# Optimization experiments

Measured on AMD Instinct MI355X. Metric: run time of the kernel, lower is better.

Reference implementation:

```python
import jax, jax.numpy as jnp
import numpy as np

DIM = 2048        # model hidden size
INTER = 1408      # per-expert intermediate size
E = 16            # n_routed_experts
TOPK = 2          # n_activated_experts
S_INTER = 2816    # shared experts intermediate (n_shared_experts * INTER)
T = 4096          # tokens (batch*seq, module flattens to [-1, dim])
ROUTE_SCALE = 1.0


def setup_inputs() -> dict:
    key = jax.random.key(0)
    ks = jax.random.split(key, 8)
    g = lambda k, shape, scale: (jax.random.normal(k, shape, dtype=jnp.float32) * scale)
    return {
        "x": g(ks[0], (T, DIM), 1.0),
        "gate_w": g(ks[1], (E, DIM), 0.02),
        "w1": g(ks[2], (E, INTER, DIM), 0.02),
        "w2": g(ks[3], (E, DIM, INTER), 0.02),
        "w3": g(ks[4], (E, INTER, DIM), 0.02),
        "sw1": g(ks[5], (S_INTER, DIM), 0.02),
        "sw2": g(ks[6], (DIM, S_INTER), 0.02),
        "sw3": g(ks[7], (S_INTER, DIM), 0.02),
    }


def _moe_forward(x, gate_w, w1, w2, w3, sw1, sw2, sw3):
    t = x.shape[0]
    # ---- gate: softmax scores -> top-k experts per token ----
    scores = jax.nn.softmax(x @ gate_w.T, axis=-1)          # [T, E]
    top_w, top_i = jax.lax.top_k(scores, TOPK)              # [T, K]
    top_w = top_w * ROUTE_SCALE
    # dense combine weights [T, E]: zero for unselected experts
    combine = jnp.zeros((t, E), x.dtype).at[jnp.arange(t)[:, None], top_i].add(top_w)
    # ---- routed experts: gated silu MLP per expert, weighted combine ----
    # loop over the small fixed expert count; tokens with combine==0 contribute 0,
    # matching the original scatter/gather dispatch math exactly.
    y = jnp.zeros_like(x)
    for e in range(E):
        h = jax.nn.silu(x @ w1[e].T) * (x @ w3[e].T)        # [T, INTER]
        y = y + (h @ w2[e].T) * combine[:, e:e + 1]
    # ---- shared experts ----
    z = (jax.nn.silu(x @ sw1.T) * (x @ sw3.T)) @ sw2.T      # [T, DIM]
    return y + z


def reference(x, gate_w, w1, w2, w3, sw1, sw2, sw3):
    return _moe_forward(x, gate_w, w1, w2, w3, sw1, sw2, sw3)
```

## Files before the change

kernel.cpp:

```cpp
#include <hip/hip_runtime.h>
#include <hip/hip_bf16.h>
#include <cstdint>
#include <cstddef>

#define TTOK   4096
#define DIM_   2048
#define INTER_ 1408
#define NEXP   16
#define SINTER_ 2816
#define BM 128
#define BN 128
#define BK 32
#define MAXROWS (TTOK*2 + NEXP*BM)
#define MAXMT   (TTOK*2/BM + NEXP)

typedef unsigned short u16;
typedef __attribute__((ext_vector_type(8))) short short8;
typedef __attribute__((ext_vector_type(4))) float f32x4;

#define AS3P(p) ((__attribute__((address_space(3))) void*)(p))
#define AS1P(p) ((const __attribute__((address_space(1))) void*)(p))

__device__ __forceinline__ void gll16(const void* g, void* l) {
    __builtin_amdgcn_global_load_lds(AS1P(g), AS3P(l), 16, 0, 0);
}

__device__ __forceinline__ u16 f2bf(float f) {
    __hip_bfloat16 h = __float2bfloat16(f);
    union { __hip_bfloat16 h; u16 u; } c; c.h = h; return c.u;
}

__device__ __forceinline__ unsigned pk2(float a, float b) {
    unsigned r;
    asm("v_cvt_pk_bf16_f32 %0, %1, %2" : "=v"(r) : "v"(a), "v"(b));
    return r;
}

__device__ __forceinline__ int4 pack8(float4 a, float4 b) {
    int4 r;
    r.x = (int)pk2(a.x, a.y);
    r.y = (int)pk2(a.z, a.w);
    r.z = (int)pk2(b.x, b.y);
    r.w = (int)pk2(b.z, b.w);
    return r;
}


__global__ void init_kernel(int* perm_rt, float* pw_rt, int* perm_sh, int* misc, int* zrow) {
    int i = blockIdx.x * 256 + threadIdx.x;
    if (i < MAXROWS) { perm_rt[i] = -1; pw_rt[i] = 0.f; }
    if (i < TTOK)    perm_sh[i] = i;
    if (i < 32)      misc[i] = 0;
    if (i < 1024)    zrow[i] = 0;
}

__global__ void cvt_kernel(const float* __restrict__ s, u16* __restrict__ d, int n8) {
    int stride = gridDim.x * 256;
    for (int i = blockIdx.x * 256 + threadIdx.x; i < n8; i += stride) {
        const float4* s4 = (const float4*)(s + (size_t)i * 8);
        float4 a = s4[0], b = s4[1];
        *(int4*)(d + (size_t)i * 8) = pack8(a, b);
    }
}

__global__ void gate_kernel(const float* __restrict__ x, const float* __restrict__ gw,
                            int* __restrict__ topi, float* __restrict__ topw,
                            int* __restrict__ misc) {
    int t = blockIdx.x;
    int lane = threadIdx.x;
    const float* xr = x + (size_t)t * DIM_;
    float acc[NEXP];
#pragma unroll
    for (int e = 0; e < NEXP; e++) acc[e] = 0.f;
#pragma unroll
    for (int i = 0; i < 8; i++) {
        int k = i * 256 + lane * 4;
        float4 xv = *(const float4*)(xr + k);
#pragma unroll
        for (int e = 0; e < NEXP; e++) {
            float4 gv = *(const float4*)(gw + (size_t)e * DIM_ + k);
            acc[e] += xv.x * gv.x + xv.y * gv.y + xv.z * gv.z + xv.w * gv.w;
        }
    }
#pragma unroll
    for (int e = 0; e < NEXP; e++) {
        float v = acc[e];
        for (int off = 32; off > 0; off >>= 1) v += __shfl_down(v, off);
        acc[e] = v;
    }
    if (lane == 0) {
        float m = acc[0];
#pragma unroll
        for (int e = 1; e < NEXP; e++) m = fmaxf(m, acc[e]);
        float p[NEXP]; float s = 0.f;
#pragma unroll
        for (int e = 0; e < NEXP; e++) { p[e] = __expf(acc[e] - m); s += p[e]; }
        int i0 = 0; float v0 = p[0];
#pragma unroll
        for (int e = 1; e < NEXP; e++) if (p[e] > v0) { v0 = p[e]; i0 = e; }
        int i1 = -1; float v1 = -1.f;
#pragma unroll
        for (int e = 0; e < NEXP; e++) if (e != i0 && p[e] > v1) { v1 = p[e]; i1 = e; }
        float inv = 1.f / s;
        topi[2 * t] = i0; topi[2 * t + 1] = i1;
        topw[2 * t] = v0 * inv; topw[2 * t + 1] = v1 * inv;
        atomicAdd(&misc[i0], 1);
        atomicAdd(&misc[i1], 1);
    }
}

__global__ void scan_kernel(int* misc) {
    int* counts = misc;
    int* base   = misc + 32;
    int* te     = misc + 48;
    int* tr     = misc + 128;
    int b = 0, tt = 0;
    for (int e = 0; e < NEXP; e++) {
        int c = counts[e];
        int nt = (c + BM - 1) >> 7;
        base[e] = b;
        for (int i = 0; i < nt; i++) { te[tt] = e; tr[tt] = b + i * BM; tt++; }
        b += nt * BM;
    }
    for (int i = tt; i < MAXMT; i++) te[i] = -1;
}

__global__ void scatter_kernel(const int* __restrict__ topi, const float* __restrict__ topw,
                               int* __restrict__ misc, int* __restrict__ perm,
                               float* __restrict__ pw) {
    int t = blockIdx.x * 256 + threadIdx.x;
    if (t >= TTOK) return;
    int* fill = misc + 16;
    int* base = misc + 32;
#pragma unroll
    for (int k = 0; k < 2; k++) {
        int e = topi[2 * t + k];
        int pos = base[e] + atomicAdd(&fill[e], 1);
        perm[pos] = t;
        pw[pos] = topw[2 * t + k];
    }
}


template<bool GROUPED>
__global__ __launch_bounds__(256, 2) void gemm_h13_k(
    const u16* __restrict__ Xb,
    const u16* __restrict__ W1b, const u16* __restrict__ W3b,
    u16* __restrict__ H,
    const int* __restrict__ perm,
    const int* __restrict__ te, const int* __restrict__ tr,
    const u16* __restrict__ zrow,
    int N, int K, int nt_m, int chunk)
{
    const int q = (blockIdx.x & 7) * chunk + (blockIdx.x >> 3);
    if (q >= nt_m * (N / BN)) return;
    const int jn = q / nt_m, im = q % nt_m;
    int e, slot0;
    if (GROUPED) { e = te[im]; if (e < 0) return; slot0 = tr[im]; }
    else         { e = 0; slot0 = im * BM; }
    const int n0 = jn * BN;
    const u16* W1 = W1b + (size_t)e * N * K;
    const u16* W3 = W3b + (size_t)e * N * K;

    __shared__ __align__(16) u16 As[BM * BK];
    __shared__ __align__(16) u16 B1s[BM * BK];
    __shared__ __align__(16) u16 B3s[BM * BK];

    const int tid = threadIdx.x;
    const int lane = tid & 63, wid = tid >> 6;
    const int wr = wid >> 1, wc = wid & 1;
    const int col = lane & 15, kg = lane >> 4;

    const int lr = lane >> 2;
    const int kb = ((lane & 3) ^ ((lane >> 3) & 3)) * 8;
    const int ar0 = wid * 32 + lr, ar1 = ar0 + 16;
    const int ta0 = perm[slot0 + ar0];
    const int ta1 = perm[slot0 + ar1];
    const u16* ga0 = (ta0 >= 0 ? Xb + (size_t)ta0 * K : zrow) + kb;
    const u16* ga1 = (ta1 >= 0 ? Xb + (size_t)ta1 * K : zrow) + kb;
    const u16* gb1a = W1 + (size_t)(n0 + ar0) * K + kb;
    const u16* gb1b = W1 + (size_t)(n0 + ar1) * K + kb;
    const u16* gb3a = W3 + (size_t)(n0 + ar0) * K + kb;
    const u16* gb3b = W3 + (size_t)(n0 + ar1) * K + kb;
    u16* la0 = As  + (wid * 32) * BK;
    u16* la1 = As  + (wid * 32 + 16) * BK;
    u16* lb1a = B1s + (wid * 32) * BK;
    u16* lb1b = B1s + (wid * 32 + 16) * BK;
    u16* lb3a = B3s + (wid * 32) * BK;
    u16* lb3b = B3s + (wid * 32 + 16) * BK;

    const int sw = (col >> 1) & 3;

    f32x4 acc1[4][4] = {};
    f32x4 acc3[4][4] = {};

    for (int k0 = 0; k0 < K; k0 += BK) {
        gll16(ga0 + k0, la0);
        gll16(ga1 + k0, la1);
        gll16(gb1a + k0, lb1a);
        gll16(gb1b + k0, lb1b);
        gll16(gb3a + k0, lb3a);
        gll16(gb3b + k0, lb3b);
        __syncthreads();

        short8 a[4];
#pragma unroll
        for (int mi = 0; mi < 4; mi++)
            a[mi] = *(const short8*)(As + (wr * 64 + mi * 16 + col) * BK + ((kg ^ sw) * 8));
#pragma unroll
        for (int ni = 0; ni < 4; ni++) {
            const int rowB = (wc * 64 + ni * 16 + col) * BK + ((kg ^ sw) * 8);
            short8 v1 = *(const short8*)(B1s + rowB);
            short8 v3 = *(const short8*)(B3s + rowB);
#pragma unroll
            for (int mi = 0; mi < 4; mi++) {
                acc1[mi][ni] = __builtin_amdgcn_mfma_f32_16x16x32_bf16(a[mi], v1, acc1[mi][ni], 0, 0, 0);
                acc3[mi][ni] = __builtin_amdgcn_mfma_f32_16x16x32_bf16(a[mi], v3, acc3[mi][ni], 0, 0, 0);
            }
        }
        __syncthreads();
    }

#pragma unroll
    for (int mi = 0; mi < 4; mi++) {
#pragma unroll
        for (int j = 0; j < 4; j++) {
            int row = slot0 + wr * 64 + mi * 16 + kg * 4 + j;
#pragma unroll
            for (int ni = 0; ni < 4; ni++) {
                float v1 = acc1[mi][ni][j];
                float v3 = acc3[mi][ni][j];
                float hv = v1 / (1.f + __expf(-v1)) * v3;
                int c = n0 + wc * 64 + ni * 16 + col;
                H[(size_t)row * N + c] = f2bf(hv);
            }
        }
    }
}

template<bool ATOMIC>
__global__ __launch_bounds__(256, 2) void gemm_out_k(
    const u16* __restrict__ Hm,
    const u16* __restrict__ W2b,
    float* __restrict__ Out,
    const int* __restrict__ perm, const float* __restrict__ pw,
    const int* __restrict__ te, const int* __restrict__ tr,
    int K, int nt_m, int chunk)
{
    const int q = (blockIdx.x & 7) * chunk + (blockIdx.x >> 3);
    if (q >= nt_m * (DIM_ / BN)) return;
    const int jn = q / nt_m, im = q % nt_m;
    int e, slot0;
    if (ATOMIC) { e = te[im]; if (e < 0) return; slot0 = tr[im]; }
    else        { e = 0; slot0 = im * BM; }
    const int n0 = jn * BN;
    const u16* W2 = W2b + (size_t)e * DIM_ * K;

    __shared__ __align__(16) u16 As[BM * BK];
    __shared__ __align__(16) u16 Bs[BM * BK];

    const int tid = threadIdx.x;
    const int lane = tid & 63, wid = tid >> 6;
    const int wr = wid >> 1, wc = wid & 1;
    const int col = lane & 15, kg = lane >> 4;

    const int lr = lane >> 2;
    const int kb = ((lane & 3) ^ ((lane >> 3) & 3)) * 8;
    const int ar0 = wid * 32 + lr, ar1 = ar0 + 16;
    const u16* ga0 = Hm + (size_t)(slot0 + ar0) * K + kb;
    const u16* ga1 = Hm + (size_t)(slot0 + ar1) * K + kb;
    const u16* gb0 = W2 + (size_t)(n0 + ar0) * K + kb;
    const u16* gb1 = W2 + (size_t)(n0 + ar1) * K + kb;
    u16* la0 = As + (wid * 32) * BK;
    u16* la1 = As + (wid * 32 + 16) * BK;
    u16* lb0 = Bs + (wid * 32) * BK;
    u16* lb1 = Bs + (wid * 32 + 16) * BK;

    const int sw = (col >> 1) & 3;

    f32x4 acc[4][4] = {};

    for (int k0 = 0; k0 < K; k0 += BK) {
        gll16(ga0 + k0, la0);
        gll16(ga1 + k0, la1);
        gll16(gb0 + k0, lb0);
        gll16(gb1 + k0, lb1);
        __syncthreads();

        short8 a[4];
#pragma unroll
        for (int mi = 0; mi < 4; mi++)
            a[mi] = *(const short8*)(As + (wr * 64 + mi * 16 + col) * BK + ((kg ^ sw) * 8));
#pragma unroll
        for (int ni = 0; ni < 4; ni++) {
            short8 bv = *(const short8*)(Bs + (wc * 64 + ni * 16 + col) * BK + ((kg ^ sw) * 8));
#pragma unroll
            for (int mi = 0; mi < 4; mi++)
                acc[mi][ni] = __builtin_amdgcn_mfma_f32_16x16x32_bf16(a[mi], bv, acc[mi][ni], 0, 0, 0);
        }
        __syncthreads();
    }

#pragma unroll
    for (int mi = 0; mi < 4; mi++) {
#pragma unroll
        for (int j = 0; j < 4; j++) {
            int rloc = wr * 64 + mi * 16 + kg * 4 + j;
            int slot = slot0 + rloc;
            if (ATOMIC) {
                int token = perm[slot];
                if (token < 0) continue;
                float w = pw[slot];
#pragma unroll
                for (int ni = 0; ni < 4; ni++) {
                    int c = n0 + wc * 64 + ni * 16 + col;
                    atomicAdd(&Out[(size_t)token * DIM_ + c], acc[mi][ni][j] * w);
                }
            } else {
#pragma unroll
                for (int ni = 0; ni < 4; ni++) {
                    int c = n0 + wc * 64 + ni * 16 + col;
                    Out[(size_t)slot * DIM_ + c] = acc[mi][ni][j];
                }
            }
        }
    }
}


extern "C" void kernel_launch(void* const* d_in, const int* in_sizes, int n_in,
                              void* d_out, int out_size, void* d_ws, size_t ws_size,
                              hipStream_t stream) {
    (void)in_sizes; (void)n_in; (void)out_size; (void)ws_size;
    const float* x   = (const float*)d_in[0];
    const float* gw  = (const float*)d_in[1];
    const float* w1  = (const float*)d_in[2];
    const float* w2  = (const float*)d_in[3];
    const float* w3  = (const float*)d_in[4];
    const float* sw1 = (const float*)d_in[5];
    const float* sw2 = (const float*)d_in[6];
    const float* sw3 = (const float*)d_in[7];
    float* out = (float*)d_out;

    char* ws = (char*)d_ws;
    size_t off = 0;
    auto take = [&](size_t bytes) -> void* {
        void* p = ws + off;
        off += (bytes + 255) & ~(size_t)255;
        return p;
    };
    u16*   xb      = (u16*)take((size_t)TTOK * DIM_ * 2);
    u16*   hbuf    = (u16*)take((size_t)MAXROWS * INTER_ * 2);
    int*   perm_rt = (int*)take((size_t)MAXROWS * 4);
    float* pw_rt   = (float*)take((size_t)MAXROWS * 4);
    int*   perm_sh = (int*)take((size_t)TTOK * 4);
    int*   topi    = (int*)take((size_t)TTOK * 2 * 4);
    float* topw    = (float*)take((size_t)TTOK * 2 * 4);
    int*   misc    = (int*)take(1024);
    int*   zrow    = (int*)take(4096);
    const size_t nW  = (size_t)NEXP * INTER_ * DIM_;
    const size_t nSW = (size_t)SINTER_ * DIM_;
    u16* w1b  = (u16*)take(nW * 2);
    u16* w2b  = (u16*)take(nW * 2);
    u16* w3b  = (u16*)take(nW * 2);
    u16* sw1b = (u16*)take(nSW * 2);
    u16* sw2b = (u16*)take(nSW * 2);
    u16* sw3b = (u16*)take(nSW * 2);

    init_kernel<<<MAXROWS / 256, 256, 0, stream>>>(perm_rt, pw_rt, perm_sh, misc, zrow);
    cvt_kernel<<<2048, 256, 0, stream>>>(x, xb, TTOK * DIM_ / 8);
    gate_kernel<<<TTOK, 64, 0, stream>>>(x, gw, topi, topw, misc);
    scan_kernel<<<1, 1, 0, stream>>>(misc);
    scatter_kernel<<<TTOK / 256, 256, 0, stream>>>(topi, topw, misc, perm_rt, pw_rt);

    cvt_kernel<<<4096, 256, 0, stream>>>(w1,  w1b,  (int)(nW / 8));
    cvt_kernel<<<4096, 256, 0, stream>>>(w2,  w2b,  (int)(nW / 8));
    cvt_kernel<<<4096, 256, 0, stream>>>(w3,  w3b,  (int)(nW / 8));
    cvt_kernel<<<4096, 256, 0, stream>>>(sw1, sw1b, (int)(nSW / 8));
    cvt_kernel<<<4096, 256, 0, stream>>>(sw2, sw2b, (int)(nSW / 8));
    cvt_kernel<<<4096, 256, 0, stream>>>(sw3, sw3b, (int)(nSW / 8));

    auto grid8 = [](int total) { return ((total + 7) / 8) * 8; };
    auto chunk8 = [](int total) { return (total + 7) / 8; };

    {
        int total = (TTOK / BM) * (SINTER_ / BN);
        gemm_h13_k<false><<<grid8(total), 256, 0, stream>>>(
            xb, sw1b, sw3b, hbuf, perm_sh, nullptr, nullptr, (const u16*)zrow,
            SINTER_, DIM_, TTOK / BM, chunk8(total));
    }
    {
        int total = (TTOK / BM) * (DIM_ / BN);
        gemm_out_k<false><<<grid8(total), 256, 0, stream>>>(
            hbuf, sw2b, out, nullptr, nullptr, nullptr, nullptr,
            SINTER_, TTOK / BM, chunk8(total));
    }
    {
        int total = MAXMT * (INTER_ / BN);
        gemm_h13_k<true><<<grid8(total), 256, 0, stream>>>(
            xb, w1b, w3b, hbuf, perm_rt, misc + 48, misc + 128, (const u16*)zrow,
            INTER_, DIM_, MAXMT, chunk8(total));
    }
    {
        int total = MAXMT * (DIM_ / BN);
        gemm_out_k<true><<<grid8(total), 256, 0, stream>>>(
            hbuf, w2b, out, perm_rt, pw_rt, misc + 48, misc + 128,
            INTER_, MAXMT, chunk8(total));
    }
}
```

Before: 864.0 us.

## Split fused W1/W3 gate GEMM into two single-B GEMMs with bf16 intermediate

```diff
diff --git a/kernel.cpp b/kernel.cpp
--- a/kernel.cpp
+++ b/kernel.cpp
@@ -30,6 +30,10 @@
     union { __hip_bfloat16 h; u16 u; } c; c.h = h; return c.u;
 }
 
+__device__ __forceinline__ float bf2f(u16 u) {
+    return __uint_as_float((unsigned)u << 16);
+}
+
 __device__ __forceinline__ unsigned pk2(float a, float b) {
     unsigned r;
     asm("v_cvt_pk_bf16_f32 %0, %1, %2" : "=v"(r) : "v"(a), "v"(b));
@@ -46,10 +50,9 @@
 }
 
 
-__global__ void init_kernel(int* perm_rt, float* pw_rt, int* perm_sh, int* misc, int* zrow) {
+__global__ void init_kernel(int* perm_rt, float* pw_rt, int* misc, int* zrow) {
     int i = blockIdx.x * 256 + threadIdx.x;
     if (i < MAXROWS) { perm_rt[i] = -1; pw_rt[i] = 0.f; }
-    if (i < TTOK)    perm_sh[i] = i;
     if (i < 32)      misc[i] = 0;
     if (i < 1024)    zrow[i] = 0;
 }
@@ -142,12 +145,11 @@
 }
 
 
-template<bool GROUPED>
-__global__ __launch_bounds__(256, 2) void gemm_h13_k(
-    const u16* __restrict__ Xb,
-    const u16* __restrict__ W1b, const u16* __restrict__ W3b,
-    u16* __restrict__ H,
-    const int* __restrict__ perm,
+template<bool GROUPED, int EPI>
+__global__ __launch_bounds__(256, 3) void gemm_s(
+    const u16* __restrict__ A, const u16* __restrict__ B,
+    const u16* __restrict__ T1, u16* __restrict__ OutB, float* __restrict__ OutF,
+    const int* __restrict__ perm, const float* __restrict__ pw,
     const int* __restrict__ te, const int* __restrict__ tr,
     const u16* __restrict__ zrow,
     int N, int K, int nt_m, int chunk)
@@ -159,12 +161,10 @@
     if (GROUPED) { e = te[im]; if (e < 0) return; slot0 = tr[im]; }
     else         { e = 0; slot0 = im * BM; }
     const int n0 = jn * BN;
-    const u16* W1 = W1b + (size_t)e * N * K;
-    const u16* W3 = W3b + (size_t)e * N * K;
+    const u16* Bw = B + (size_t)e * N * K;
 
     __shared__ __align__(16) u16 As[BM * BK];
-    __shared__ __align__(16) u16 B1s[BM * BK];
-    __shared__ __align__(16) u16 B3s[BM * BK];
+    __shared__ __align__(16) u16 Bs[BM * BK];
 
     const int tid = threadIdx.x;
     const int lane = tid & 63, wid = tid >> 6;
@@ -174,103 +174,19 @@
     const int lr = lane >> 2;
     const int kb = ((lane & 3) ^ ((lane >> 3) & 3)) * 8;
     const int ar0 = wid * 32 + lr, ar1 = ar0 + 16;
-    const int ta0 = perm[slot0 + ar0];
-    const int ta1 = perm[slot0 + ar1];
-    const u16* ga0 = (ta0 >= 0 ? Xb + (size_t)ta0 * K : zrow) + kb;
-    const u16* ga1 = (ta1 >= 0 ? Xb + (size_t)ta1 * K : zrow) + kb;
-    const u16* gb1a = W1 + (size_t)(n0 + ar0) * K + kb;
-    const u16* gb1b = W1 + (size_t)(n0 + ar1) * K + kb;
-    const u16* gb3a = W3 + (size_t)(n0 + ar0) * K + kb;
-    const u16* gb3b = W3 + (size_t)(n0 + ar1) * K + kb;
-    u16* la0 = As  + (wid * 32) * BK;
-    u16* la1 = As  + (wid * 32 + 16) * BK;
-    u16* lb1a = B1s + (wid * 32) * BK;
-    u16* lb1b = B1s + (wid * 32 + 16) * BK;
-    u16* lb3a = B3s + (wid * 32) * BK;
-    u16* lb3b = B3s + (wid * 32 + 16) * BK;
-
-    const int sw = (col >> 1) & 3;
-
-    f32x4 acc1[4][4] = {};
-    f32x4 acc3[4][4] = {};
-
-    for (int k0 = 0; k0 < K; k0 += BK) {
-        gll16(ga0 + k0, la0);
-        gll16(ga1 + k0, la1);
-        gll16(gb1a + k0, lb1a);
-        gll16(gb1b + k0, lb1b);
-        gll16(gb3a + k0, lb3a);
-        gll16(gb3b + k0, lb3b);
-        __syncthreads();
-
-        short8 a[4];
-#pragma unroll
-        for (int mi = 0; mi < 4; mi++)
-            a[mi] = *(const short8*)(As + (wr * 64 + mi * 16 + col) * BK + ((kg ^ sw) * 8));
-#pragma unroll
-        for (int ni = 0; ni < 4; ni++) {
-            const int rowB = (wc * 64 + ni * 16 + col) * BK + ((kg ^ sw) * 8);
-            short8 v1 = *(const short8*)(B1s + rowB);
-            short8 v3 = *(const short8*)(B3s + rowB);
-#pragma unroll
-            for (int mi = 0; mi < 4; mi++) {
-                acc1[mi][ni] = __builtin_amdgcn_mfma_f32_16x16x32_bf16(a[mi], v1, acc1[mi][ni], 0, 0, 0);
-                acc3[mi][ni] = __builtin_amdgcn_mfma_f32_16x16x32_bf16(a[mi], v3, acc3[mi][ni], 0, 0, 0);
-            }
-        }
-        __syncthreads();
-    }
-
-#pragma unroll
-    for (int mi = 0; mi < 4; mi++) {
-#pragma unroll
-        for (int j = 0; j < 4; j++) {
-            int row = slot0 + wr * 64 + mi * 16 + kg * 4 + j;
-#pragma unroll
-            for (int ni = 0; ni < 4; ni++) {
-                float v1 = acc1[mi][ni][j];
-                float v3 = acc3[mi][ni][j];
-                float hv = v1 / (1.f + __expf(-v1)) * v3;
-                int c = n0 + wc * 64 + ni * 16 + col;
-                H[(size_t)row * N + c] = f2bf(hv);
-            }
-        }
-    }
-}
-
-template<bool ATOMIC>
-__global__ __launch_bounds__(256, 2) void gemm_out_k(
-    const u16* __restrict__ Hm,
-    const u16* __restrict__ W2b,
-    float* __restrict__ Out,
-    const int* __restrict__ perm, const float* __restrict__ pw,
-    const int* __restrict__ te, const int* __restrict__ tr,
-    int K, int nt_m, int chunk)
-{
-    const int q = (blockIdx.x & 7) * chunk + (blockIdx.x >> 3);
-    if (q >= nt_m * (DIM_ / BN)) return;
-    const int jn = q / nt_m, im = q % nt_m;
-    int e, slot0;
-    if (ATOMIC) { e = te[im]; if (e < 0) return; slot0 = tr[im]; }
-    else        { e = 0; slot0 = im * BM; }
-    const int n0 = jn * BN;
-    const u16* W2 = W2b + (size_t)e * DIM_ * K;
-
-    __shared__ __align__(16) u16 As[BM * BK];
-    __shared__ __align__(16) u16 Bs[BM * BK];
-
-    const int tid = threadIdx.x;
-    const int lane = tid & 63, wid = tid >> 6;
-    const int wr = wid >> 1, wc = wid & 1;
-    const int col = lane & 15, kg = lane >> 4;
-
-    const int lr = lane >> 2;
-    const int kb = ((lane & 3) ^ ((lane >> 3) & 3)) * 8;
-    const int ar0 = wid * 32 + lr, ar1 = ar0 + 16;
-    const u16* ga0 = Hm + (size_t)(slot0 + ar0) * K + kb;
-    const u16* ga1 = Hm + (size_t)(slot0 + ar1) * K + kb;
-    const u16* gb0 = W2 + (size_t)(n0 + ar0) * K + kb;
-    const u16* gb1 = W2 + (size_t)(n0 + ar1) * K + kb;
+    const u16* ga0;
+    const u16* ga1;
+    if (GROUPED && EPI < 2) {
+        const int ta0 = perm[slot0 + ar0];
+        const int ta1 = perm[slot0 + ar1];
+        ga0 = (ta0 >= 0 ? A + (size_t)ta0 * K : zrow) + kb;
+        ga1 = (ta1 >= 0 ? A + (size_t)ta1 * K : zrow) + kb;
+    } else {
+        ga0 = A + (size_t)(slot0 + ar0) * K + kb;
+        ga1 = A + (size_t)(slot0 + ar1) * K + kb;
+    }
+    const u16* gb0 = Bw + (size_t)(n0 + ar0) * K + kb;
+    const u16* gb1 = Bw + (size_t)(n0 + ar1) * K + kb;
     u16* la0 = As + (wid * 32) * BK;
     u16* la1 = As + (wid * 32 + 16) * BK;
     u16* lb0 = Bs + (wid * 32) * BK;
@@ -307,20 +223,35 @@
         for (int j = 0; j < 4; j++) {
             int rloc = wr * 64 + mi * 16 + kg * 4 + j;
             int slot = slot0 + rloc;
-            if (ATOMIC) {
+            if (EPI == 0) {
+#pragma unroll
+                for (int ni = 0; ni < 4; ni++) {
+                    float v = acc[mi][ni][j];
+                    float s = v / (1.f + __expf(-v));
+                    int c = n0 + wc * 64 + ni * 16 + col;
+                    OutB[(size_t)slot * N + c] = f2bf(s);
+                }
+            } else if (EPI == 1) {
+#pragma unroll
+                for (int ni = 0; ni < 4; ni++) {
+                    int c = n0 + wc * 64 + ni * 16 + col;
+                    float s1 = bf2f(T1[(size_t)slot * N + c]);
+                    OutB[(size_t)slot * N + c] = f2bf(s1 * acc[mi][ni][j]);
+                }
+            } else if (EPI == 2) {
+#pragma unroll
+                for (int ni = 0; ni < 4; ni++) {
+                    int c = n0 + wc * 64 + ni * 16 + col;
+                    OutF[(size_t)slot * DIM_ + c] = acc[mi][ni][j];
+                }
+            } else {
                 int token = perm[slot];
                 if (token < 0) continue;
                 float w = pw[slot];
 #pragma unroll
                 for (int ni = 0; ni < 4; ni++) {
                     int c = n0 + wc * 64 + ni * 16 + col;
-                    atomicAdd(&Out[(size_t)token * DIM_ + c], acc[mi][ni][j] * w);
-                }
-            } else {
-#pragma unroll
-                for (int ni = 0; ni < 4; ni++) {
-                    int c = n0 + wc * 64 + ni * 16 + col;
-                    Out[(size_t)slot * DIM_ + c] = acc[mi][ni][j];
+                    atomicAdd(&OutF[(size_t)token * DIM_ + c], acc[mi][ni][j] * w);
                 }
             }
         }
@@ -349,11 +280,13 @@
         off += (bytes + 255) & ~(size_t)255;
         return p;
     };
+    const size_t nT1 = (size_t)MAXROWS * INTER_;
+    const size_t nHB = (nT1 > (size_t)TTOK * SINTER_) ? nT1 : (size_t)TTOK * SINTER_;
     u16*   xb      = (u16*)take((size_t)TTOK * DIM_ * 2);
-    u16*   hbuf    = (u16*)take((size_t)MAXROWS * INTER_ * 2);
+    u16*   t1buf   = (u16*)take(nHB * 2);
+    u16*   hbuf    = (u16*)take(nHB * 2);
     int*   perm_rt = (int*)take((size_t)MAXROWS * 4);
     float* pw_rt   = (float*)take((size_t)MAXROWS * 4);
-    int*   perm_sh = (int*)take((size_t)TTOK * 4);
     int*   topi    = (int*)take((size_t)TTOK * 2 * 4);
     float* topw    = (float*)take((size_t)TTOK * 2 * 4);
     int*   misc    = (int*)take(1024);
@@ -367,7 +300,7 @@
     u16* sw2b = (u16*)take(nSW * 2);
     u16* sw3b = (u16*)take(nSW * 2);
 
-    init_kernel<<<MAXROWS / 256, 256, 0, stream>>>(perm_rt, pw_rt, perm_sh, misc, zrow);
+    init_kernel<<<MAXROWS / 256, 256, 0, stream>>>(perm_rt, pw_rt, misc, zrow);
     cvt_kernel<<<2048, 256, 0, stream>>>(x, xb, TTOK * DIM_ / 8);
     gate_kernel<<<TTOK, 64, 0, stream>>>(x, gw, topi, topw, misc);
     scan_kernel<<<1, 1, 0, stream>>>(misc);
@@ -383,28 +316,36 @@
     auto grid8 = [](int total) { return ((total + 7) / 8) * 8; };
     auto chunk8 = [](int total) { return (total + 7) / 8; };
 
+    const int ntm_sh = TTOK / BM;
+
     {
-        int total = (TTOK / BM) * (SINTER_ / BN);
-        gemm_h13_k<false><<<grid8(total), 256, 0, stream>>>(
-            xb, sw1b, sw3b, hbuf, perm_sh, nullptr, nullptr, (const u16*)zrow,
-            SINTER_, DIM_, TTOK / BM, chunk8(total));
+        int total = ntm_sh * (SINTER_ / BN);
+        gemm_s<false, 0><<<grid8(total), 256, 0, stream>>>(
+            xb, sw1b, nullptr, t1buf, nullptr, nullptr, nullptr, nullptr, nullptr,
+            (const u16*)zrow, SINTER_, DIM_, ntm_sh, chunk8(total));
+        gemm_s<false, 1><<<grid8(total), 256, 0, stream>>>(
+            xb, sw3b, t1buf, hbuf, nullptr, nullptr, nullptr, nullptr, nullptr,
+            (const u16*)zrow, SINTER_, DIM_, ntm_sh, chunk8(total));
     }
     {
-        int total = (TTOK / BM) * (DIM_ / BN);
-        gemm_out_k<false><<<grid8(total), 256, 0, stream>>>(
-            hbuf, sw2b, out, nullptr, nullptr, nullptr, nullptr,
-            SINTER_, TTOK / BM, chunk8(total));
+        int total = ntm_sh * (DIM_ / BN);
+        gemm_s<false, 2><<<grid8(total), 256, 0, stream>>>(
+            hbuf, sw2b, nullptr, nullptr, out, nullptr, nullptr, nullptr, nullptr,
+            (const u16*)zrow, DIM_, SINTER_, ntm_sh, chunk8(total));
     }
     {
         int total = MAXMT * (INTER_ / BN);
-        gemm_h13_k<true><<<grid8(total), 256, 0, stream>>>(
-            xb, w1b, w3b, hbuf, perm_rt, misc + 48, misc + 128, (const u16*)zrow,
-            INTER_, DIM_, MAXMT, chunk8(total));
+        gemm_s<true, 0><<<grid8(total), 256, 0, stream>>>(
+            xb, w1b, nullptr, t1buf, nullptr, perm_rt, nullptr, misc + 48, misc + 128,
+            (const u16*)zrow, INTER_, DIM_, MAXMT, chunk8(total));
+        gemm_s<true, 1><<<grid8(total), 256, 0, stream>>>(
+            xb, w3b, t1buf, hbuf, nullptr, perm_rt, nullptr, misc + 48, misc + 128,
+            (const u16*)zrow, INTER_, DIM_, MAXMT, chunk8(total));
     }
     {
         int total = MAXMT * (DIM_ / BN);
-        gemm_out_k<true><<<grid8(total), 256, 0, stream>>>(
-            hbuf, w2b, out, perm_rt, pw_rt, misc + 48, misc + 128,
-            INTER_, MAXMT, chunk8(total));
-    }
-}
+        gemm_s<true, 3><<<grid8(total), 256, 0, stream>>>(
+            hbuf, w2b, nullptr, nullptr, out, perm_rt, pw_rt, misc + 48, misc + 128,
+            (const u16*)zrow, DIM_, INTER_, MAXMT, chunk8(total));
+    }
+}
```

New measurement: 876.4 us. No clear change (+1.4%).
